# Performance work log

Measured on AMD Instinct MI355X. Metric: run time of the kernel, lower is better.

The kernel has to match this reference:

```python
import jax, jax.numpy as jnp
import numpy as np

WIDTH, HEIGHT = 256, 256
FOV = 1.0471975511965976  # 60 deg horizontal fov, radians
Z_NEAR, Z_FAR = 2.0, 6.0
NUM_SAMPLES = 64
HIDDEN = 64


def get_cam_ray_dirs(width, height, horizontal_fov):
    rot_y = jnp.linspace(-horizontal_fov / 2.0, horizontal_fov / 2.0, width)
    vfov = horizontal_fov * height / width
    rot_x = jnp.linspace(vfov / 2.0, -vfov / 2.0, height)
    rot_y = jnp.broadcast_to(rot_y[None, :], (height, width))
    rot_x = jnp.broadcast_to(rot_x[:, None], (height, width))
    x = -jnp.sin(rot_y) * jnp.cos(rot_x)
    y = jnp.sin(rot_x)
    z = -jnp.cos(rot_y) * jnp.cos(rot_x)
    return jnp.stack([x, y, z], axis=2)  # (H, W, 3)


def setup_inputs() -> dict:
    key = jax.random.key(0)
    k1, k2, k3, k4, k5 = jax.random.split(key, 5)
    camera_local_to_world = jax.random.normal(k1, (4, 4), dtype=jnp.float32)
    u = jax.random.uniform(k2, (HEIGHT * WIDTH, NUM_SAMPLES), dtype=jnp.float32)
    cam_ray_dirs = get_cam_ray_dirs(WIDTH, HEIGHT, FOV).astype(jnp.float32)
    W1 = jax.random.normal(k3, (6, HIDDEN), dtype=jnp.float32) * 0.4
    b1 = jnp.zeros((HIDDEN,), dtype=jnp.float32)
    W2 = jax.random.normal(k4, (HIDDEN, 4), dtype=jnp.float32) * 0.1
    b2 = jnp.zeros((4,), dtype=jnp.float32)
    return {"camera_local_to_world": camera_local_to_world, "u": u,
            "cam_ray_dirs": cam_ray_dirs, "W1": W1, "b1": b1, "W2": W2, "b2": b2}


def reference(camera_local_to_world, u, cam_ray_dirs, W1, b1, W2, b2):
    H, W, _ = cam_ray_dirs.shape
    R = H * W
    S = u.shape[1]

    # world-space rays
    rot = camera_local_to_world[:3, :3]
    ray_origin = camera_local_to_world[:3, 3]                    # (3,)
    ray_dirs = jnp.einsum('ij,hwj->hwi', rot, cam_ray_dirs).reshape(R, 3)

    # binned-uniform sample distances along each ray
    dt = Z_FAR - Z_NEAR
    bin_dt = dt / S
    t = jnp.linspace(Z_NEAR, Z_FAR - bin_dt, S, dtype=jnp.float32)[None, :] + u * bin_dt  # (R, S)

    # sample positions and view directions
    pos = ray_origin[None, None, :] + ray_dirs[:, None, :] * t[:, :, None]   # (R, S, 3)
    dirs = jnp.broadcast_to(ray_dirs[:, None, :], (R, S, 3))
    x = jnp.concatenate([pos.reshape(R * S, 3), dirs.reshape(R * S, 3)], axis=1)  # (R*S, 6)

    # radiance MLP: density (non-negative) + rgb color
    h = jax.nn.relu(x @ W1 + b1)                 # (R*S, HIDDEN)
    out = h @ W2 + b2                            # (R*S, 4)
    densities = jax.nn.relu(out[:, 0]).reshape(R, S)
    colors = jax.nn.sigmoid(out[:, 1:]).reshape(R, S, 3)

    # alpha compositing (vectorized form of the back-to-front recurrence:
    # weight_i = alpha_i * prod_{j<i}(1 - alpha_j))
    seps = t[:, 1:] - t[:, :-1]                                   # (R, S-1)
    alphas = 1.0 - jnp.exp(-densities[:, :-1] * seps)             # (R, S-1)
    last_alpha = 1.0 - jnp.exp(-densities[:, -1:] * bin_dt)       # mean_sample_separation = bin_dt
    a = jnp.concatenate([alphas, last_alpha], axis=1)             # (R, S)
    trans = jnp.cumprod(1.0 - a, axis=1)
    T = jnp.concatenate([jnp.ones((R, 1), a.dtype), trans[:, :-1]], axis=1)  # exclusive cumprod
    weights = a * T                                               # (R, S)
    color = jnp.sum(weights[:, :, None] * colors, axis=1)         # (R, 3)
    return color.reshape(H, W, 3)
```

## Files before the change

### kernel.cpp

```cpp
#include <hip/hip_runtime.h>

#define NUM_SAMPLES 64
#define HIDDEN 64
#define Z_NEAR 2.0f
#define Z_FAR 6.0f
#define LOG2E 1.44269504088896f

typedef _Float16 half8 __attribute__((ext_vector_type(8)));
typedef __fp16  fp16x2 __attribute__((ext_vector_type(2)));
typedef float   float4t __attribute__((ext_vector_type(4)));

template<int CTRL, int RMASK>
__device__ __forceinline__ float dpp_add(float x) {
    const int m = __builtin_amdgcn_update_dpp(0, __float_as_int(x), CTRL, RMASK, 0xf, true);
    return x + __int_as_float(m);
}
__device__ __forceinline__ float wave_scan_add(float x) {
    x = dpp_add<0x111, 0xf>(x);
    x = dpp_add<0x112, 0xf>(x);
    x = dpp_add<0x114, 0xf>(x);
    x = dpp_add<0x118, 0xf>(x);
    x = dpp_add<0x142, 0xa>(x);
    x = dpp_add<0x143, 0xc>(x);
    return x;
}

__device__ __forceinline__ int slot16(int s) { return 2*s + ((s>>2)&1); }

__global__ __launch_bounds__(256) void render_kernel(
    const float* __restrict__ cam,
    const float* __restrict__ u,
    const float* __restrict__ cdirs,
    const float* __restrict__ W1,
    const float* __restrict__ b1,
    const float* __restrict__ W2,
    const float* __restrict__ b2,
    float* __restrict__ out)
{
    const int lane = threadIdx.x & 63;
    const int wid  = threadIdx.x >> 6;
    const int ray  = blockIdx.x * 4 + wid;
    const int grp  = lane >> 4;
    const int col  = lane & 15;

    __shared__ __align__(16) __fp16 Ahsh[4][HIDDEN];
    __shared__ __align__(16) __fp16 Bhsh[4][HIDDEN];
    __shared__ __align__(16) float  tsh[4][NUM_SAMPLES];
    __shared__ __align__(16) __fp16 W2T[4][4][80];
    __shared__ __align__(16) float  cst[4][NUM_SAMPLES*8];

    {
        const float4 w2row = ((const float4*)W2)[lane];
        W2T[wid][0][lane] = (__fp16)w2row.x;
        W2T[wid][1][lane] = (__fp16)w2row.y;
        W2T[wid][2][lane] = (__fp16)w2row.z;
        W2T[wid][3][lane] = (__fp16)w2row.w;
    }

    const float cd0 = cdirs[ray*3+0], cd1 = cdirs[ray*3+1], cd2 = cdirs[ray*3+2];
    const float rd0 = fmaf(cam[0], cd0, fmaf(cam[1], cd1, cam[2]*cd2));
    const float rd1 = fmaf(cam[4], cd0, fmaf(cam[5], cd1, cam[6]*cd2));
    const float rd2 = fmaf(cam[8], cd0, fmaf(cam[9], cd1, cam[10]*cd2));
    const float o0 = cam[3], o1 = cam[7], o2 = cam[11];

    {
        const int h = lane;
        const float w10 = W1[0*HIDDEN+h], w11 = W1[1*HIDDEN+h], w12 = W1[2*HIDDEN+h];
        const float w13 = W1[3*HIDDEN+h], w14 = W1[4*HIDDEN+h], w15 = W1[5*HIDDEN+h];
        const float A = fmaf(rd0, w10, fmaf(rd1, w11, rd2*w12));
        float B = fmaf(o0, w10, fmaf(o1, w11, o2*w12));
        B = fmaf(rd0, w13, fmaf(rd1, w14, fmaf(rd2, w15, B))) + b1[h];
        Ahsh[wid][lane] = (__fp16)A;
        Bhsh[wid][lane] = (__fp16)B;
    }

    const float bin_dt = (Z_FAR - Z_NEAR) / (float)NUM_SAMPLES;
    const float uv = u[ray*NUM_SAMPLES + lane];
    const float t  = fmaf((float)lane + uv, bin_dt, Z_NEAR);
    tsh[wid][lane] = t;

    union { fp16x2 h2[4]; half8 h8; } aAh[2], aBh[2];
    #pragma unroll
    for (int kt = 0; kt < 2; ++kt) {
        const int h0 = kt*32 + grp*8;
        aAh[kt].h8 = *(const half8*)(&Ahsh[wid][h0]);
        aBh[kt].h8 = *(const half8*)(&Bhsh[wid][h0]);
    }

    half8 bfrag[2] = {};
    if (col < 4) {
        bfrag[0] = *(const half8*)(&W2T[wid][col][grp*8]);
        bfrag[1] = *(const half8*)(&W2T[wid][col][32 + grp*8]);
    }
    const float b20 = b2[0], b21 = b2[1], b22 = b2[2], b23 = b2[3];

    const float tn  = tsh[wid][(lane+1) & 63];
    const float sep = (lane < NUM_SAMPLES-1) ? (tn - t) : bin_dt;

    const fp16x2 hzero = {(__fp16)0.0f, (__fp16)0.0f};

    #pragma unroll
    for (int m = 0; m < 4; ++m) {
        const float tm = tsh[wid][col + 16*m];
        const fp16x2 tvh = __builtin_amdgcn_cvt_pkrtz(tm, tm);
        float4t c = {0.f, 0.f, 0.f, 0.f};
        #pragma unroll
        for (int kt = 0; kt < 2; ++kt) {
            union { fp16x2 h2[4]; half8 h8; } au;
            #pragma unroll
            for (int q = 0; q < 4; ++q) {
                const fp16x2 pre = __builtin_elementwise_fma(aAh[kt].h2[q], tvh, aBh[kt].h2[q]);
                au.h2[q] = __builtin_elementwise_max(pre, hzero);
            }
            c = __builtin_amdgcn_mfma_f32_16x16x32_f16(bfrag[kt], au.h8, c, 0, 0, 0);
        }
        if (lane < 16)
            *(float4t*)(&cst[wid][slot16(16*m + lane) * 4]) = c;
    }

    const float4t c4 = *(const float4t*)(&cst[wid][slot16(lane) * 4]);
    const float acc0 = c4[0] + b20;
    const float acc1 = c4[1] + b21;
    const float acc2 = c4[2] + b22;
    const float acc3 = c4[3] + b23;

    const float density = fmaxf(acc0, 0.0f);
    const float dsep  = density * sep;
    const float lg    = -dsep * LOG2E;
    const float alpha = 1.0f - __builtin_amdgcn_exp2f(lg);
    const float S     = wave_scan_add(lg);
    const float T     = __builtin_amdgcn_exp2f(S - lg);
    const float w     = alpha * T;

    float c0 = w * __builtin_amdgcn_rcpf(1.0f + __builtin_amdgcn_exp2f(-acc1 * LOG2E));
    float c1 = w * __builtin_amdgcn_rcpf(1.0f + __builtin_amdgcn_exp2f(-acc2 * LOG2E));
    float c2 = w * __builtin_amdgcn_rcpf(1.0f + __builtin_amdgcn_exp2f(-acc3 * LOG2E));
    c0 = wave_scan_add(c0);
    c1 = wave_scan_add(c1);
    c2 = wave_scan_add(c2);
    if (lane == 63) {
        out[ray*3+0] = c0;
        out[ray*3+1] = c1;
        out[ray*3+2] = c2;
    }
}

extern "C" void kernel_launch(void* const* d_in, const int* in_sizes, int n_in,
                              void* d_out, int out_size, void* d_ws, size_t ws_size,
                              hipStream_t stream) {
    const float* cam   = (const float*)d_in[0];
    const float* u     = (const float*)d_in[1];
    const float* cdirs = (const float*)d_in[2];
    const float* W1    = (const float*)d_in[3];
    const float* b1    = (const float*)d_in[4];
    const float* W2    = (const float*)d_in[5];
    const float* b2    = (const float*)d_in[6];
    float* out = (float*)d_out;

    const int R = 256 * 256;
    dim3 grid(R / 4), block(256);
    render_kernel<<<grid, block, 0, stream>>>(cam, u, cdirs, W1, b1, W2, b2, out);
}
```

Baseline: 28.19 us.

## Process two rays per wavefront with t recomputed from u instead of LDS

Each wavefront now renders two rays instead of one, and the grid is halved. All global loads (u, cdirs, W1, b1, b2) are hoisted up front, and the per-block W2 transpose and setup are amortized over twice the work. Sample distances are recomputed directly from u values loaded per lane rather than exchanged through a shared t array. This trades more registers and redundant global loads of u for fewer blocks and less LDS traffic and setup per ray.

```diff
diff --git a/kernel.cpp b/kernel.cpp
--- a/kernel.cpp
+++ b/kernel.cpp
@@ -39,13 +39,15 @@
 {
     const int lane = threadIdx.x & 63;
     const int wid  = threadIdx.x >> 6;
-    const int ray  = blockIdx.x * 4 + wid;
     const int grp  = lane >> 4;
     const int col  = lane & 15;
-
-    __shared__ __align__(16) __fp16 Ahsh[4][HIDDEN];
-    __shared__ __align__(16) __fp16 Bhsh[4][HIDDEN];
-    __shared__ __align__(16) float  tsh[4][NUM_SAMPLES];
+    const int rayA = blockIdx.x * 8 + wid * 2;
+    const int rayB = rayA + 1;
+
+    __shared__ __align__(16) __fp16 AhshA[4][HIDDEN];
+    __shared__ __align__(16) __fp16 BhshA[4][HIDDEN];
+    __shared__ __align__(16) __fp16 AhshB[4][HIDDEN];
+    __shared__ __align__(16) __fp16 BhshB[4][HIDDEN];
     __shared__ __align__(16) __fp16 W2T[4][4][80];
     __shared__ __align__(16) float  cst[4][NUM_SAMPLES*8];
 
@@ -57,34 +59,43 @@
         W2T[wid][3][lane] = (__fp16)w2row.w;
     }
 
-    const float cd0 = cdirs[ray*3+0], cd1 = cdirs[ray*3+1], cd2 = cdirs[ray*3+2];
-    const float rd0 = fmaf(cam[0], cd0, fmaf(cam[1], cd1, cam[2]*cd2));
-    const float rd1 = fmaf(cam[4], cd0, fmaf(cam[5], cd1, cam[6]*cd2));
-    const float rd2 = fmaf(cam[8], cd0, fmaf(cam[9], cd1, cam[10]*cd2));
+    const float* upA = u + rayA*NUM_SAMPLES;
+    const float* upB = u + rayB*NUM_SAMPLES;
+    const int lnext = (lane < 63) ? lane+1 : 63;
+    const float uvA  = upA[lane];
+    const float uvAn = upA[lnext];
+    const float uA0 = upA[col], uA1 = upA[16+col], uA2 = upA[32+col], uA3 = upA[48+col];
+    const float uvB  = upB[lane];
+    const float uvBn = upB[lnext];
+    const float uB0 = upB[col], uB1 = upB[16+col], uB2 = upB[32+col], uB3 = upB[48+col];
+
+    const float cdA0 = cdirs[rayA*3+0], cdA1 = cdirs[rayA*3+1], cdA2 = cdirs[rayA*3+2];
+    const float cdB0 = cdirs[rayB*3+0], cdB1 = cdirs[rayB*3+1], cdB2 = cdirs[rayB*3+2];
+
+    const float w10 = W1[0*HIDDEN+lane], w11 = W1[1*HIDDEN+lane], w12 = W1[2*HIDDEN+lane];
+    const float w13 = W1[3*HIDDEN+lane], w14 = W1[4*HIDDEN+lane], w15 = W1[5*HIDDEN+lane];
+    const float b1h = b1[lane];
+    const float b20 = b2[0], b21 = b2[1], b22 = b2[2], b23 = b2[3];
     const float o0 = cam[3], o1 = cam[7], o2 = cam[11];
 
     {
-        const int h = lane;
-        const float w10 = W1[0*HIDDEN+h], w11 = W1[1*HIDDEN+h], w12 = W1[2*HIDDEN+h];
-        const float w13 = W1[3*HIDDEN+h], w14 = W1[4*HIDDEN+h], w15 = W1[5*HIDDEN+h];
-        const float A = fmaf(rd0, w10, fmaf(rd1, w11, rd2*w12));
-        float B = fmaf(o0, w10, fmaf(o1, w11, o2*w12));
-        B = fmaf(rd0, w13, fmaf(rd1, w14, fmaf(rd2, w15, B))) + b1[h];
-        Ahsh[wid][lane] = (__fp16)A;
-        Bhsh[wid][lane] = (__fp16)B;
-    }
-
-    const float bin_dt = (Z_FAR - Z_NEAR) / (float)NUM_SAMPLES;
-    const float uv = u[ray*NUM_SAMPLES + lane];
-    const float t  = fmaf((float)lane + uv, bin_dt, Z_NEAR);
-    tsh[wid][lane] = t;
-
-    union { fp16x2 h2[4]; half8 h8; } aAh[2], aBh[2];
-    #pragma unroll
-    for (int kt = 0; kt < 2; ++kt) {
-        const int h0 = kt*32 + grp*8;
-        aAh[kt].h8 = *(const half8*)(&Ahsh[wid][h0]);
-        aBh[kt].h8 = *(const half8*)(&Bhsh[wid][h0]);
+        const float rdA0 = fmaf(cam[0], cdA0, fmaf(cam[1], cdA1, cam[2]*cdA2));
+        const float rdA1 = fmaf(cam[4], cdA0, fmaf(cam[5], cdA1, cam[6]*cdA2));
+        const float rdA2 = fmaf(cam[8], cdA0, fmaf(cam[9], cdA1, cam[10]*cdA2));
+        const float AA = fmaf(rdA0, w10, fmaf(rdA1, w11, rdA2*w12));
+        float BA = fmaf(o0, w10, fmaf(o1, w11, o2*w12));
+        BA = fmaf(rdA0, w13, fmaf(rdA1, w14, fmaf(rdA2, w15, BA))) + b1h;
+        AhshA[wid][lane] = (__fp16)AA;
+        BhshA[wid][lane] = (__fp16)BA;
+
+        const float rdB0 = fmaf(cam[0], cdB0, fmaf(cam[1], cdB1, cam[2]*cdB2));
+        const float rdB1 = fmaf(cam[4], cdB0, fmaf(cam[5], cdB1, cam[6]*cdB2));
+        const float rdB2 = fmaf(cam[8], cdB0, fmaf(cam[9], cdB1, cam[10]*cdB2));
+        const float AB = fmaf(rdB0, w10, fmaf(rdB1, w11, rdB2*w12));
+        float BB = fmaf(o0, w10, fmaf(o1, w11, o2*w12));
+        BB = fmaf(rdB0, w13, fmaf(rdB1, w14, fmaf(rdB2, w15, BB))) + b1h;
+        AhshB[wid][lane] = (__fp16)AB;
+        BhshB[wid][lane] = (__fp16)BB;
     }
 
     half8 bfrag[2] = {};
@@ -92,56 +103,122 @@
         bfrag[0] = *(const half8*)(&W2T[wid][col][grp*8]);
         bfrag[1] = *(const half8*)(&W2T[wid][col][32 + grp*8]);
     }
-    const float b20 = b2[0], b21 = b2[1], b22 = b2[2], b23 = b2[3];
-
-    const float tn  = tsh[wid][(lane+1) & 63];
-    const float sep = (lane < NUM_SAMPLES-1) ? (tn - t) : bin_dt;
-
+
+    const float bin_dt = (Z_FAR - Z_NEAR) / (float)NUM_SAMPLES;
     const fp16x2 hzero = {(__fp16)0.0f, (__fp16)0.0f};
-
-    #pragma unroll
-    for (int m = 0; m < 4; ++m) {
-        const float tm = tsh[wid][col + 16*m];
-        const fp16x2 tvh = __builtin_amdgcn_cvt_pkrtz(tm, tm);
-        float4t c = {0.f, 0.f, 0.f, 0.f};
+    union u8t { fp16x2 h2[4]; half8 h8; };
+
+    float resA0, resA1, resA2, resB0, resB1, resB2;
+
+    {
+        u8t aAh[2], aBh[2];
         #pragma unroll
         for (int kt = 0; kt < 2; ++kt) {
-            union { fp16x2 h2[4]; half8 h8; } au;
+            const int h0 = kt*32 + grp*8;
+            aAh[kt].h8 = *(const half8*)(&AhshA[wid][h0]);
+            aBh[kt].h8 = *(const half8*)(&BhshA[wid][h0]);
+        }
+        const float t   = fmaf((float)lane + uvA, bin_dt, Z_NEAR);
+        const float tn  = fmaf((float)(lane+1) + uvAn, bin_dt, Z_NEAR);
+        const float sep = (lane < NUM_SAMPLES-1) ? (tn - t) : bin_dt;
+
+        #pragma unroll
+        for (int m = 0; m < 4; ++m) {
+            const float um = (m==0) ? uA0 : (m==1) ? uA1 : (m==2) ? uA2 : uA3;
+            const float tm = fmaf((float)(16*m + col) + um, bin_dt, Z_NEAR);
+            const fp16x2 tvh = __builtin_amdgcn_cvt_pkrtz(tm, tm);
+            float4t c = {0.f, 0.f, 0.f, 0.f};
             #pragma unroll
-            for (int q = 0; q < 4; ++q) {
-                const fp16x2 pre = __builtin_elementwise_fma(aAh[kt].h2[q], tvh, aBh[kt].h2[q]);
-                au.h2[q] = __builtin_elementwise_max(pre, hzero);
+            for (int kt = 0; kt < 2; ++kt) {
+                u8t au;
+                #pragma unroll
+                for (int q = 0; q < 4; ++q) {
+                    const fp16x2 pre = __builtin_elementwise_fma(aAh[kt].h2[q], tvh, aBh[kt].h2[q]);
+                    au.h2[q] = __builtin_elementwise_max(pre, hzero);
+                }
+                c = __builtin_amdgcn_mfma_f32_16x16x32_f16(bfrag[kt], au.h8, c, 0, 0, 0);
             }
-            c = __builtin_amdgcn_mfma_f32_16x16x32_f16(bfrag[kt], au.h8, c, 0, 0, 0);
-        }
-        if (lane < 16)
-            *(float4t*)(&cst[wid][slot16(16*m + lane) * 4]) = c;
-    }
-
-    const float4t c4 = *(const float4t*)(&cst[wid][slot16(lane) * 4]);
-    const float acc0 = c4[0] + b20;
-    const float acc1 = c4[1] + b21;
-    const float acc2 = c4[2] + b22;
-    const float acc3 = c4[3] + b23;
-
-    const float density = fmaxf(acc0, 0.0f);
-    const float dsep  = density * sep;
-    const float lg    = -dsep * LOG2E;
-    const float alpha = 1.0f - __builtin_amdgcn_exp2f(lg);
-    const float S     = wave_scan_add(lg);
-    const float T     = __builtin_amdgcn_exp2f(S - lg);
-    const float w     = alpha * T;
-
-    float c0 = w * __builtin_amdgcn_rcpf(1.0f + __builtin_amdgcn_exp2f(-acc1 * LOG2E));
-    float c1 = w * __builtin_amdgcn_rcpf(1.0f + __builtin_amdgcn_exp2f(-acc2 * LOG2E));
-    float c2 = w * __builtin_amdgcn_rcpf(1.0f + __builtin_amdgcn_exp2f(-acc3 * LOG2E));
-    c0 = wave_scan_add(c0);
-    c1 = wave_scan_add(c1);
-    c2 = wave_scan_add(c2);
+            if (lane < 16)
+                *(float4t*)(&cst[wid][slot16(16*m + lane) * 4]) = c;
+        }
+
+        const float4t c4 = *(const float4t*)(&cst[wid][slot16(lane) * 4]);
+        const float acc0 = c4[0] + b20, acc1 = c4[1] + b21;
+        const float acc2 = c4[2] + b22, acc3 = c4[3] + b23;
+
+        const float dsep  = fmaxf(acc0, 0.0f) * sep;
+        const float lg    = -dsep * LOG2E;
+        const float alpha = 1.0f - __builtin_amdgcn_exp2f(lg);
+        const float S     = wave_scan_add(lg);
+        const float T     = __builtin_amdgcn_exp2f(S - lg);
+        const float w     = alpha * T;
+
+        float c0 = w * __builtin_amdgcn_rcpf(1.0f + __builtin_amdgcn_exp2f(-acc1 * LOG2E));
+        float c1 = w * __builtin_amdgcn_rcpf(1.0f + __builtin_amdgcn_exp2f(-acc2 * LOG2E));
+        float c2 = w * __builtin_amdgcn_rcpf(1.0f + __builtin_amdgcn_exp2f(-acc3 * LOG2E));
+        resA0 = wave_scan_add(c0);
+        resA1 = wave_scan_add(c1);
+        resA2 = wave_scan_add(c2);
+    }
+
+    {
+        u8t aAh[2], aBh[2];
+        #pragma unroll
+        for (int kt = 0; kt < 2; ++kt) {
+            const int h0 = kt*32 + grp*8;
+            aAh[kt].h8 = *(const half8*)(&AhshB[wid][h0]);
+            aBh[kt].h8 = *(const half8*)(&BhshB[wid][h0]);
+        }
+        const float t   = fmaf((float)lane + uvB, bin_dt, Z_NEAR);
+        const float tn  = fmaf((float)(lane+1) + uvBn, bin_dt, Z_NEAR);
+        const float sep = (lane < NUM_SAMPLES-1) ? (tn - t) : bin_dt;
+
+        #pragma unroll
+        for (int m = 0; m < 4; ++m) {
+            const float um = (m==0) ? uB0 : (m==1) ? uB1 : (m==2) ? uB2 : uB3;
+            const float tm = fmaf((float)(16*m + col) + um, bin_dt, Z_NEAR);
+            const fp16x2 tvh = __builtin_amdgcn_cvt_pkrtz(tm, tm);
+            float4t c = {0.f, 0.f, 0.f, 0.f};
+            #pragma unroll
+            for (int kt = 0; kt < 2; ++kt) {
+                u8t au;
+                #pragma unroll
+                for (int q = 0; q < 4; ++q) {
+                    const fp16x2 pre = __builtin_elementwise_fma(aAh[kt].h2[q], tvh, aBh[kt].h2[q]);
+                    au.h2[q] = __builtin_elementwise_max(pre, hzero);
+                }
+                c = __builtin_amdgcn_mfma_f32_16x16x32_f16(bfrag[kt], au.h8, c, 0, 0, 0);
+            }
+            if (lane < 16)
+                *(float4t*)(&cst[wid][slot16(16*m + lane) * 4]) = c;
+        }
+
+        const float4t c4 = *(const float4t*)(&cst[wid][slot16(lane) * 4]);
+        const float acc0 = c4[0] + b20, acc1 = c4[1] + b21;
+        const float acc2 = c4[2] + b22, acc3 = c4[3] + b23;
+
+        const float dsep  = fmaxf(acc0, 0.0f) * sep;
+        const float lg    = -dsep * LOG2E;
+        const float alpha = 1.0f - __builtin_amdgcn_exp2f(lg);
+        const float S     = wave_scan_add(lg);
+        const float T     = __builtin_amdgcn_exp2f(S - lg);
+        const float w     = alpha * T;
+
+        float c0 = w * __builtin_amdgcn_rcpf(1.0f + __builtin_amdgcn_exp2f(-acc1 * LOG2E));
+        float c1 = w * __builtin_amdgcn_rcpf(1.0f + __builtin_amdgcn_exp2f(-acc2 * LOG2E));
+        float c2 = w * __builtin_amdgcn_rcpf(1.0f + __builtin_amdgcn_exp2f(-acc3 * LOG2E));
+        resB0 = wave_scan_add(c0);
+        resB1 = wave_scan_add(c1);
+        resB2 = wave_scan_add(c2);
+    }
+
     if (lane == 63) {
-        out[ray*3+0] = c0;
-        out[ray*3+1] = c1;
-        out[ray*3+2] = c2;
+        out[rayA*3+0] = resA0;
+        out[rayA*3+1] = resA1;
+        out[rayA*3+2] = resA2;
+        out[rayB*3+0] = resB0;
+        out[rayB*3+1] = resB1;
+        out[rayB*3+2] = resB2;
     }
 }
 
@@ -158,6 +235,6 @@
     float* out = (float*)d_out;
 
     const int R = 256 * 256;
-    dim3 grid(R / 4), block(256);
+    dim3 grid(R / 8), block(256);
     render_kernel<<<grid, block, 0, stream>>>(cam, u, cdirs, W1, b1, W2, b2, out);
 }
```

After: 29.02 us. +3.0%, slower.

## Keep MFMA outputs in registers and composite per 16-lane row

Applied to the files above, without the earlier changes.

The MFMA accumulators are no longer staged through shared memory and redistributed one sample per lane. Each lane now keeps its four accumulator tiles in registers. Transmittance comes from 16-lane row scans stitched together with readlane offsets, and colours are accumulated per lane before a final row scan. This removes the LDS store/load round-trip and the cross-row DPP steps. In exchange, each lane does four times the transcendental work, since only lanes in rows holding valid columns carry useful data and the remaining rows compute redundantly.

```diff
diff --git a/kernel.cpp b/kernel.cpp
--- a/kernel.cpp
+++ b/kernel.cpp
@@ -15,17 +15,13 @@
     const int m = __builtin_amdgcn_update_dpp(0, __float_as_int(x), CTRL, RMASK, 0xf, true);
     return x + __int_as_float(m);
 }
-__device__ __forceinline__ float wave_scan_add(float x) {
+__device__ __forceinline__ float row_scan_add(float x) {
     x = dpp_add<0x111, 0xf>(x);
     x = dpp_add<0x112, 0xf>(x);
     x = dpp_add<0x114, 0xf>(x);
     x = dpp_add<0x118, 0xf>(x);
-    x = dpp_add<0x142, 0xa>(x);
-    x = dpp_add<0x143, 0xc>(x);
     return x;
 }
-
-__device__ __forceinline__ int slot16(int s) { return 2*s + ((s>>2)&1); }
 
 __global__ __launch_bounds__(256) void render_kernel(
     const float* __restrict__ cam,
@@ -47,7 +43,6 @@
     __shared__ __align__(16) __fp16 Bhsh[4][HIDDEN];
     __shared__ __align__(16) float  tsh[4][NUM_SAMPLES];
     __shared__ __align__(16) __fp16 W2T[4][4][80];
-    __shared__ __align__(16) float  cst[4][NUM_SAMPLES*8];
 
     {
         const float4 w2row = ((const float4*)W2)[lane];
@@ -94,15 +89,15 @@
     }
     const float b20 = b2[0], b21 = b2[1], b22 = b2[2], b23 = b2[3];
 
-    const float tn  = tsh[wid][(lane+1) & 63];
-    const float sep = (lane < NUM_SAMPLES-1) ? (tn - t) : bin_dt;
-
     const fp16x2 hzero = {(__fp16)0.0f, (__fp16)0.0f};
 
+    float4t cacc[4];
+    float   tm[4], tnx[4];
     #pragma unroll
     for (int m = 0; m < 4; ++m) {
-        const float tm = tsh[wid][col + 16*m];
-        const fp16x2 tvh = __builtin_amdgcn_cvt_pkrtz(tm, tm);
+        tm[m]  = tsh[wid][col + 16*m];
+        tnx[m] = tsh[wid][(col + 16*m + 1) & 63];
+        const fp16x2 tvh = __builtin_amdgcn_cvt_pkrtz(tm[m], tm[m]);
         float4t c = {0.f, 0.f, 0.f, 0.f};
         #pragma unroll
         for (int kt = 0; kt < 2; ++kt) {
@@ -114,34 +109,51 @@
             }
             c = __builtin_amdgcn_mfma_f32_16x16x32_f16(bfrag[kt], au.h8, c, 0, 0, 0);
         }
-        if (lane < 16)
-            *(float4t*)(&cst[wid][slot16(16*m + lane) * 4]) = c;
+        cacc[m] = c;
     }
 
-    const float4t c4 = *(const float4t*)(&cst[wid][slot16(lane) * 4]);
-    const float acc0 = c4[0] + b20;
-    const float acc1 = c4[1] + b21;
-    const float acc2 = c4[2] + b22;
-    const float acc3 = c4[3] + b23;
+    float lg[4], alpha[4];
+    #pragma unroll
+    for (int m = 0; m < 4; ++m) {
+        const float sep = (16*m + col < 63) ? (tnx[m] - tm[m]) : bin_dt;
+        const float density = fmaxf(cacc[m][0] + b20, 0.0f);
+        lg[m]    = -(density * sep) * LOG2E;
+        alpha[m] = 1.0f - __builtin_amdgcn_exp2f(lg[m]);
+    }
 
-    const float density = fmaxf(acc0, 0.0f);
-    const float dsep  = density * sep;
-    const float lg    = -dsep * LOG2E;
-    const float alpha = 1.0f - __builtin_amdgcn_exp2f(lg);
-    const float S     = wave_scan_add(lg);
-    const float T     = __builtin_amdgcn_exp2f(S - lg);
-    const float w     = alpha * T;
+    float sc[4];
+    #pragma unroll
+    for (int m = 0; m < 4; ++m) sc[m] = row_scan_add(lg[m]);
 
-    float c0 = w * __builtin_amdgcn_rcpf(1.0f + __builtin_amdgcn_exp2f(-acc1 * LOG2E));
-    float c1 = w * __builtin_amdgcn_rcpf(1.0f + __builtin_amdgcn_exp2f(-acc2 * LOG2E));
-    float c2 = w * __builtin_amdgcn_rcpf(1.0f + __builtin_amdgcn_exp2f(-acc3 * LOG2E));
-    c0 = wave_scan_add(c0);
-    c1 = wave_scan_add(c1);
-    c2 = wave_scan_add(c2);
-    if (lane == 63) {
-        out[ray*3+0] = c0;
-        out[ray*3+1] = c1;
-        out[ray*3+2] = c2;
+    const float tot0 = __int_as_float(__builtin_amdgcn_readlane(__float_as_int(sc[0]), 15));
+    const float tot1 = __int_as_float(__builtin_amdgcn_readlane(__float_as_int(sc[1]), 15));
+    const float tot2 = __int_as_float(__builtin_amdgcn_readlane(__float_as_int(sc[2]), 15));
+    const float off1 = tot0, off2 = tot0 + tot1, off3 = off2 + tot2;
+
+    float w[4];
+    w[0] = alpha[0] * __builtin_amdgcn_exp2f(sc[0]          - lg[0]);
+    w[1] = alpha[1] * __builtin_amdgcn_exp2f(sc[1] + off1   - lg[1]);
+    w[2] = alpha[2] * __builtin_amdgcn_exp2f(sc[2] + off2   - lg[2]);
+    w[3] = alpha[3] * __builtin_amdgcn_exp2f(sc[3] + off3   - lg[3]);
+
+    float p0 = 0.f, p1 = 0.f, p2 = 0.f;
+    #pragma unroll
+    for (int m = 0; m < 4; ++m) {
+        const float s1 = __builtin_amdgcn_rcpf(1.0f + __builtin_amdgcn_exp2f(-(cacc[m][1] + b21) * LOG2E));
+        const float s2 = __builtin_amdgcn_rcpf(1.0f + __builtin_amdgcn_exp2f(-(cacc[m][2] + b22) * LOG2E));
+        const float s3 = __builtin_amdgcn_rcpf(1.0f + __builtin_amdgcn_exp2f(-(cacc[m][3] + b23) * LOG2E));
+        p0 = fmaf(w[m], s1, p0);
+        p1 = fmaf(w[m], s2, p1);
+        p2 = fmaf(w[m], s3, p2);
+    }
+    p0 = row_scan_add(p0);
+    p1 = row_scan_add(p1);
+    p2 = row_scan_add(p2);
+
+    if (lane == 15) {
+        out[ray*3+0] = p0;
+        out[ray*3+1] = p1;
+        out[ray*3+2] = p2;
     }
 }
 
```

Result: slower. 39.70 us (+40.8%).
